# Optimization experiments

Hardware: AMD Instinct MI355X
Metric: run time of the kernel (lower is better)

The kernel has to match this reference:

```python
import jax, jax.numpy as jnp
import numpy as np
from jax import lax


def conv2d(x, w, pad):
    return lax.conv_general_dilated(x, w, (1, 1), [(pad, pad), (pad, pad)],
                                    dimension_numbers=('NCHW', 'OIHW', 'NCHW'))


def deform_conv2d(x, offset, w, b, k, pad):
    # torchvision-style DeformConv2d, stride 1, dilation 1, 1 group.
    # offset: [B, 2*k*k, H, W], pairs ordered (dy, dx) per kernel tap (row-major).
    B, C, H, W = x.shape
    KK = k * k
    off = offset.reshape(B, KK, 2, H, W)
    ky, kx = jnp.meshgrid(jnp.arange(k), jnp.arange(k), indexing='ij')
    ky = ky.reshape(1, KK, 1, 1).astype(x.dtype)
    kx = kx.reshape(1, KK, 1, 1).astype(x.dtype)
    gy = jnp.arange(H, dtype=x.dtype).reshape(1, 1, H, 1)
    gx = jnp.arange(W, dtype=x.dtype).reshape(1, 1, 1, W)
    ys = gy + ky - pad + off[:, :, 0]  # [B, KK, H, W]
    xs = gx + kx - pad + off[:, :, 1]
    y0 = jnp.floor(ys)
    x0 = jnp.floor(xs)
    y1 = y0 + 1.0
    x1 = x0 + 1.0
    img = x.reshape(B, C, H * W)

    def corner(yc, xc, wt):
        # zero padding outside the image
        valid = (yc >= 0) & (yc <= H - 1) & (xc >= 0) & (xc <= W - 1)
        idx = (jnp.clip(yc, 0, H - 1) * W + jnp.clip(xc, 0, W - 1)).astype(jnp.int32).reshape(B, -1)
        g = jax.vmap(lambda im, ix: jnp.take(im, ix, axis=1))(img, idx)  # [B, C, KK*H*W]
        return g.reshape(B, C, KK, H, W) * (wt * valid)[:, None]

    v = (corner(y0, x0, (y1 - ys) * (x1 - xs))
         + corner(y0, x1, (y1 - ys) * (xs - x0))
         + corner(y1, x0, (ys - y0) * (x1 - xs))
         + corner(y1, x1, (ys - y0) * (xs - x0)))  # [B, C, KK, H, W]
    out = jnp.einsum('bckhw,ock->bohw', v, w.reshape(w.shape[0], C, KK))
    return out + b[None, :, None, None]


def setup_inputs() -> dict:
    key = jax.random.key(0)
    ks = jax.random.split(key, 16)
    f32 = jnp.float32
    dim = 64

    def rn(k, shape, s):
        return jax.random.normal(k, shape, f32) * s

    return {
        'x': rn(ks[0], (4, dim, 96, 96), 1.0),
        'w_off3': rn(ks[1], (18, dim, 3, 3), 0.01), 'b_off3': jnp.zeros((18,), f32),
        'w_off5': rn(ks[2], (50, dim, 3, 3), 0.01), 'b_off5': jnp.zeros((50,), f32),
        'w_off7': rn(ks[3], (98, dim, 3, 3), 0.01), 'b_off7': jnp.zeros((98,), f32),
        'w_d3': rn(ks[4], (dim, dim, 3, 3), 0.04), 'b_d3': rn(ks[5], (dim,), 0.01),
        'w_d5': rn(ks[6], (dim, dim, 5, 5), 0.025), 'b_d5': rn(ks[7], (dim,), 0.01),
        'w_d7': rn(ks[8], (dim, dim, 7, 7), 0.018), 'b_d7': rn(ks[9], (dim,), 0.01),
        'w_sp': rn(ks[10], (1, 2, 7, 7), 0.1),
        'w_ca1': rn(ks[11], (12, 3 * dim, 1, 1), 0.07),
        'w_ca2': rn(ks[12], (3 * dim, 12, 1, 1), 0.28),
    }


def reference(x, w_off3, b_off3, w_off5, b_off5, w_off7, b_off7,
              w_d3, b_d3, w_d5, b_d5, w_d7, b_d7, w_sp, w_ca1, w_ca2):
    off3 = conv2d(x, w_off3, 1) + b_off3[None, :, None, None]
    off5 = conv2d(x, w_off5, 1) + b_off5[None, :, None, None]
    off7 = conv2d(x, w_off7, 1) + b_off7[None, :, None, None]
    a1 = deform_conv2d(x, off3, w_d3, b_d3, 3, 1)
    a2 = deform_conv2d(x, off5, w_d5, b_d5, 5, 2)
    a3 = deform_conv2d(x, off7, w_d7, b_d7, 7, 3)
    res = jnp.concatenate([a1, a2, a3], axis=1)  # [B, 3C, H, W]

    # SpatialAttention: channel mean/max -> 7x7 conv -> sigmoid
    sp_in = jnp.concatenate([jnp.mean(res, axis=1, keepdims=True),
                             jnp.max(res, axis=1, keepdims=True)], axis=1)
    sp = jax.nn.sigmoid(conv2d(sp_in, w_sp, 3))  # [B, 1, H, W]

    # ChannelAttention: shared MLP on avg- and max-pooled descriptors
    def fc(t):
        return conv2d(jnp.maximum(conv2d(t, w_ca1, 0), 0.0), w_ca2, 0)

    avg = jnp.mean(res, axis=(2, 3), keepdims=True)
    mx = jnp.max(res, axis=(2, 3), keepdims=True)
    ch = jax.nn.sigmoid(fc(avg) + fc(mx))  # [B, 3C, 1, 1]

    C = x.shape[1]
    c1, c2, c3 = ch[:, :C], ch[:, C:2 * C], ch[:, 2 * C:]
    return a1 * (sp + c1) + a2 * (sp + c2) + a3 * (sp + c3)
```

## Files before the change

### kernel.cpp

```cpp
#include <hip/hip_runtime.h>
#include <math.h>

#define H 96
#define W 96
#define HW (H*W)
#define CIN 64
#define NB 4
#define NOFF 166
#define OFFROW 168

typedef __attribute__((ext_vector_type(8)))  short short8;
typedef __attribute__((ext_vector_type(8)))  _Float16 half8;
typedef __attribute__((ext_vector_type(16))) float f32x16;
typedef unsigned short ushort_t;

static const size_t OFF_ALL = 0;
static const size_t RES     = OFF_ALL + (size_t)NB*HW*OFFROW;
static const size_t XB16    = RES + (size_t)NB*192*HW;
static const size_t WTD3    = XB16 + (size_t)NB*64*HW/2;
static const size_t WTD5    = WTD3 + 9*4096/2;
static const size_t WTD7    = WTD5 + 25*4096/2;
static const size_t WOFF    = WTD7 + 49*4096/2;
static const size_t BOFF    = WOFF + 9*192*64/2;
static const size_t SPIN    = BOFF + 192;
static const size_t SPATT   = SPIN + (size_t)NB*2*HW;
static const size_t POOLAVG = SPATT + (size_t)NB*HW;
static const size_t POOLMAX = POOLAVG + NB*192;
static const size_t CHATT   = POOLMAX + NB*192;

__device__ __forceinline__ ushort_t f2h(float f) {
    _Float16 h = (_Float16)f;
    return __builtin_bit_cast(unsigned short, h);
}
__device__ __forceinline__ half8 as_h8(short8 s) {
    return __builtin_bit_cast(half8, s);
}
__device__ __forceinline__ half8 splat8(float f) {
    _Float16 h = (_Float16)f;
    half8 v;
    #pragma unroll
    for (int j = 0; j < 8; j++) v[j] = h;
    return v;
}

__global__ __launch_bounds__(256) void convert_x_nhwc_kernel(const float* __restrict__ x,
                                                             ushort_t* __restrict__ xb) {
    __shared__ ushort_t tile[64][66];
    int t = threadIdx.x;
    int b = blockIdx.x / 144;
    int p0 = (blockIdx.x % 144) * 64;
    int q = t >> 6, ln = t & 63;
    #pragma unroll
    for (int i = 0; i < 16; i++) {
        int c = q * 16 + i;
        tile[ln][c] = f2h(x[((size_t)(b * 64 + c)) * HW + p0 + ln]);
    }
    __syncthreads();
    #pragma unroll
    for (int i = 0; i < 16; i++) {
        int pos = q * 16 + i;
        xb[((size_t)b * HW + p0 + pos) * 64 + ln] = tile[pos][ln];
    }
}

__global__ void convert_weights_kernel(const float* __restrict__ w3, const float* __restrict__ w5,
                                       const float* __restrict__ w7,
                                       const float* __restrict__ ob3, const float* __restrict__ ob5,
                                       const float* __restrict__ ob7,
                                       const float* __restrict__ ow3, const float* __restrict__ ow5,
                                       const float* __restrict__ ow7,
                                       ushort_t* __restrict__ wt3, ushort_t* __restrict__ wt5,
                                       ushort_t* __restrict__ wt7,
                                       ushort_t* __restrict__ woff, float* __restrict__ boff) {
    int idx = blockIdx.x * 256 + threadIdx.x;
    if (idx < 83 * 4096) {
        const float* src; ushort_t* dst; int KK; int o;
        if (idx < 9 * 4096)       { src = w3; dst = wt3; KK = 9;  o = idx; }
        else if (idx < 34 * 4096) { src = w5; dst = wt5; KK = 25; o = idx - 9 * 4096; }
        else                      { src = w7; dst = wt7; KK = 49; o = idx - 34 * 4096; }
        int j    = o & 7;
        int l31  = (o >> 3) & 31;
        int lh   = (o >> 8) & 1;
        int cs   = (o >> 9) & 3;
        int half = (o >> 11) & 1;
        int kk   = o >> 12;
        int co = half * 32 + l31;
        int c  = cs * 16 + lh * 8 + j;
        dst[o] = f2h(src[((size_t)co * 64 + c) * KK + kk]);
        return;
    }
    int o = idx - 83 * 4096;
    if (o >= 9 * 192 * 64) return;
    int c  = o & 63;
    int co = (o >> 6) % 192;
    int kk = o / (192 * 64);
    float v = 0.f;
    if (co < 18)       v = ow3[(co * 64 + c) * 9 + kk];
    else if (co < 68)  v = ow5[((co - 18) * 64 + c) * 9 + kk];
    else if (co < 166) v = ow7[((co - 68) * 64 + c) * 9 + kk];
    woff[(kk * 192 + co) * 64 + c] = f2h(v);
    if (kk == 0 && c == 0) {
        float bv = 0.f;
        if (co < 18)       bv = ob3[co];
        else if (co < 68)  bv = ob5[co - 18];
        else if (co < 166) bv = ob7[co - 68];
        boff[co] = bv;
    }
}

__global__ __launch_bounds__(256, 3) void offset_mfma_kernel(
    const ushort_t* __restrict__ xb,
    const ushort_t* __restrict__ woff,
    const float* __restrict__ bias_all,
    float* __restrict__ off_all)
{
    __shared__ float red[6144];
    const int t = threadIdx.x;
    const int lane = t & 63, l31 = lane & 31, lh = lane >> 5;
    const int wave = t >> 6;
    const int mhalf = wave >> 1, khalf = wave & 1;
    const int xcd = blockIdx.x & 7, u = blockIdx.x >> 3;
    const int b = xcd >> 1;
    const int v = u * 2 + (xcd & 1);
    const int npos = v * 32 + l31;
    const int h = npos / 96, w = npos % 96;
    const int c0 = 8 * lh;
    const ushort_t* xbase = xb + (size_t)b * HW * 64;

    f32x16 acc0, acc1, acc2;
    #pragma unroll
    for (int r = 0; r < 16; r++) { acc0[r] = 0.f; acc1[r] = 0.f; acc2[r] = 0.f; }

    const int kk0 = khalf ? 5 : 0, kk1 = khalf ? 9 : 5;
    const int mt0 = mhalf * 3;
    for (int kk = kk0; kk < kk1; kk++) {
        int ky = kk / 3, kx = kk % 3;
        int y = h + ky - 1, x = w + kx - 1;
        bool ok = ((unsigned)y < (unsigned)H) && ((unsigned)x < (unsigned)W);
        int o = ok ? (y * W + x) : 0;
        short zm = ok ? (short)0xFFFF : (short)0;
        const ushort_t* px = xbase + (size_t)o * 64 + c0;
        const ushort_t* wk = woff + (size_t)kk * 12288;
        #pragma unroll
        for (int cs = 0; cs < 4; cs++) {
            int cc = cs * 16;
            short8 q = *(const short8*)(px + cc);
            short8 bm;
            #pragma unroll
            for (int j = 0; j < 8; j++) bm[j] = (short)(q[j] & zm);
            half8 bfrag = as_h8(bm);
            half8 a0 = as_h8(*(const short8*)(wk + (size_t)((mt0 + 0) * 32 + l31) * 64 + cc + c0));
            half8 a1 = as_h8(*(const short8*)(wk + (size_t)((mt0 + 1) * 32 + l31) * 64 + cc + c0));
            half8 a2 = as_h8(*(const short8*)(wk + (size_t)((mt0 + 2) * 32 + l31) * 64 + cc + c0));
            acc0 = __builtin_amdgcn_mfma_f32_32x32x16_f16(a0, bfrag, acc0, 0, 0, 0);
            acc1 = __builtin_amdgcn_mfma_f32_32x32x16_f16(a1, bfrag, acc1, 0, 0, 0);
            acc2 = __builtin_amdgcn_mfma_f32_32x32x16_f16(a2, bfrag, acc2, 0, 0, 0);
        }
    }

    if (khalf) {
        float* rp = red + mhalf * 3072;
        #pragma unroll
        for (int r = 0; r < 16; r++) {
            rp[(0 * 16 + r) * 64 + lane] = acc0[r];
            rp[(1 * 16 + r) * 64 + lane] = acc1[r];
            rp[(2 * 16 + r) * 64 + lane] = acc2[r];
        }
    }
    __syncthreads();
    if (!khalf) {
        const float* rp = red + mhalf * 3072;
        #pragma unroll
        for (int r = 0; r < 16; r++) {
            acc0[r] += rp[(0 * 16 + r) * 64 + lane];
            acc1[r] += rp[(1 * 16 + r) * 64 + lane];
            acc2[r] += rp[(2 * 16 + r) * 64 + lane];
        }
        float* row = off_all + ((size_t)b * HW + npos) * OFFROW;
        #pragma unroll
        for (int m = 0; m < 3; m++) {
            const f32x16& a = (m == 0) ? acc0 : (m == 1) ? acc1 : acc2;
            int mt = mt0 + m;
            #pragma unroll
            for (int q = 0; q < 4; q++) {
                int base = mt * 32 + 8 * q + 4 * lh;
                if (base < 166) {
                    float4 vv = make_float4(a[4 * q + 0] + bias_all[base + 0],
                                            a[4 * q + 1] + bias_all[base + 1],
                                            a[4 * q + 2] + bias_all[base + 2],
                                            a[4 * q + 3] + bias_all[base + 3]);
                    *(float4*)(row + base) = vv;
                }
            }
        }
    }
}

__device__ __forceinline__ void store_tile(int b, int tile, int lane, int g,
                                           const float* __restrict__ bias,
                                           const f32x16& acc0, const f32x16& acc1,
                                           float* __restrict__ res)
{
    const int l31 = lane & 31, lh = lane >> 5;
    const int npos = tile * 32 + l31;
    size_t rb = (((size_t)b * 3 + g) * 64) * HW + npos;
    #pragma unroll
    for (int r = 0; r < 16; r++) {
        int co = (r & 3) + 8 * (r >> 2) + 4 * lh;
        res[rb + (size_t)co * HW]        = acc0[r] + bias[co];
        res[rb + (size_t)(co + 32) * HW] = acc1[r] + bias[co + 32];
    }
}

#define MG  5
#define PNY 12
#define PNX 43
#define PXS 144
#define PRS (PNX * PXS)

template<int K, int PAD>
__device__ __forceinline__ void deform_span(
    const float* __restrict__ offp, const ushort_t* __restrict__ wtf,
    int kk0, int kk1, int h, int w, int w0, int l31, int lh,
    const char* lds, f32x16& acc0, f32x16& acc1)
{
    const int lh16 = lh * 16;
    const float2* offp2 = (const float2*)offp;
    float2 off = offp2[kk0];
    for (int kk = kk0; kk < kk1; kk++) {
        float2 noff = offp2[(kk + 1 < kk1) ? kk + 1 : kk];

        int ky = kk / K, kx = kk % K;
        float ys = (float)(h + ky - PAD) + off.x;
        float xs = (float)(w + kx - PAD) + off.y;
        float y0f = floorf(ys), x0f = floorf(xs);
        float fy = ys - y0f, fx = xs - x0f;
        int iy0 = (int)y0f, ix0 = (int)x0f;
        int iy1 = iy0 + 1, ix1 = ix0 + 1;
        float oky0 = ((unsigned)iy0 < (unsigned)H) ? 1.f : 0.f;
        float oky1 = ((unsigned)iy1 < (unsigned)H) ? 1.f : 0.f;
        float okx0 = ((unsigned)ix0 < (unsigned)W) ? 1.f : 0.f;
        float okx1 = ((unsigned)ix1 < (unsigned)W) ? 1.f : 0.f;
        float w00 = (1.f - fy) * (1.f - fx) * oky0 * okx0;
        float w01 = (1.f - fy) * fx * oky0 * okx1;
        float w10 = fy * (1.f - fx) * oky1 * okx0;
        float w11 = fy * fx * oky1 * okx1;
        int cy0 = min(max(iy0, 0), H - 1), cy1 = min(max(iy1, 0), H - 1);
        int cx0 = min(max(ix0, 0), W - 1), cx1 = min(max(ix1, 0), W - 1);
        int r0 = min(max(cy0 - h + MG, 0), PNY - 1);
        int r1 = min(max(cy1 - h + MG, 0), PNY - 1);
        int p0 = min(max(cx0 - w0 + MG, 0), PNX - 1);
        int p1 = min(max(cx1 - w0 + MG, 0), PNX - 1);
        const char* b00 = lds + r0 * PRS + p0 * PXS + lh16;
        const char* b01 = lds + r0 * PRS + p1 * PXS + lh16;
        const char* b10 = lds + r1 * PRS + p0 * PXS + lh16;
        const char* b11 = lds + r1 * PRS + p1 * PXS + lh16;

        half8 W00 = splat8(w00), W01 = splat8(w01);
        half8 W10 = splat8(w10), W11 = splat8(w11);
        const ushort_t* wkf = wtf + (size_t)kk * 4096;
        #pragma unroll
        for (int cs = 0; cs < 4; cs++) {
            half8 q00 = *(const half8*)(b00 + cs * 32);
            half8 q01 = *(const half8*)(b01 + cs * 32);
            half8 q10 = *(const half8*)(b10 + cs * 32);
            half8 q11 = *(const half8*)(b11 + cs * 32);
            half8 bfrag = q00 * W00 + q01 * W01 + q10 * W10 + q11 * W11;
            half8 a0 = as_h8(*(const short8*)(wkf + (size_t)(((0 * 4 + cs) * 2 + lh) * 32 + l31) * 8));
            half8 a1 = as_h8(*(const short8*)(wkf + (size_t)(((1 * 4 + cs) * 2 + lh) * 32 + l31) * 8));
            acc0 = __builtin_amdgcn_mfma_f32_32x32x16_f16(a0, bfrag, acc0, 0, 0, 0);
            acc1 = __builtin_amdgcn_mfma_f32_32x32x16_f16(a1, bfrag, acc1, 0, 0, 0);
        }
        off = noff;
    }
}

__global__ __launch_bounds__(256, 2) void deform_fused_kernel(
    const ushort_t* __restrict__ xb, const float* __restrict__ off_all,
    const ushort_t* __restrict__ wt3, const ushort_t* __restrict__ wt5,
    const ushort_t* __restrict__ wt7,
    const float* __restrict__ b3, const float* __restrict__ b5,
    const float* __restrict__ b7,
    float* __restrict__ res)
{
    __shared__ __align__(16) char lds[PNY * PNX * PXS];
    const int t = threadIdx.x;
    const int wave = t >> 6, lane = t & 63;
    const int xcd = blockIdx.x & 7, u = blockIdx.x >> 3;
    const int b = xcd >> 1;
    const int tile = u * 2 + (xcd & 1);

    const int l31 = lane & 31, lh = lane >> 5;
    const int h  = tile / 3;
    const int w0 = (tile % 3) * 32;
    const int w  = w0 + l31;
    const int npos = h * 96 + w;

    const ushort_t* xsrc = xb + (size_t)b * HW * 64;
    constexpr int NCH = PNY * PNX * 8;
    constexpr int NITER = (NCH + 255) / 256;
    #pragma unroll
    for (int it = 0; it < NITER; it++) {
        int c = t + it * 256;
        if (c < NCH) {
            int rr  = c / (PNX * 8);
            int rem = c - rr * (PNX * 8);
            int pp  = rem >> 3, sub = rem & 7;
            int cy = min(max(h - MG + rr, 0), H - 1);
            int cx = min(max(w0 - MG + pp, 0), W - 1);
            *(float4*)(lds + rr * PRS + pp * PXS + sub * 16) =
                *(const float4*)(xsrc + ((size_t)(cy * W + cx)) * 64 + sub * 8);
        }
    }
    __syncthreads();

    const float* offrow = off_all + ((size_t)b * HW + npos) * OFFROW;

    f32x16 a0A, a1A, a0B, a1B;
    #pragma unroll
    for (int r = 0; r < 16; r++) { a0A[r] = 0.f; a1A[r] = 0.f; a0B[r] = 0.f; a1B[r] = 0.f; }

    if (wave == 0) {
        deform_span<3, 1>(offrow + 0,  wt3, 0, 9,  h, w, w0, l31, lh, lds, a0A, a1A);
        deform_span<5, 2>(offrow + 18, wt5, 0, 12, h, w, w0, l31, lh, lds, a0B, a1B);
    } else if (wave == 1) {
        deform_span<5, 2>(offrow + 18, wt5, 12, 25, h, w, w0, l31, lh, lds, a0A, a1A);
        deform_span<7, 3>(offrow + 68, wt7, 0, 8,   h, w, w0, l31, lh, lds, a0B, a1B);
    } else if (wave == 2) {
        deform_span<7, 3>(offrow + 68, wt7, 8, 29,  h, w, w0, l31, lh, lds, a0A, a1A);
    } else {
        deform_span<7, 3>(offrow + 68, wt7, 29, 49, h, w, w0, l31, lh, lds, a0A, a1A);
    }

    __syncthreads();
    float* slots = (float*)lds;
    if (wave == 1) {
        float* s0 = slots;
        float* s1 = slots + 2048;
        #pragma unroll
        for (int r = 0; r < 16; r++) {
            s0[r * 64 + lane]        = a0A[r];
            s0[(16 + r) * 64 + lane] = a1A[r];
            s1[r * 64 + lane]        = a0B[r];
            s1[(16 + r) * 64 + lane] = a1B[r];
        }
    } else if (wave == 3) {
        float* s2 = slots + 4096;
        #pragma unroll
        for (int r = 0; r < 16; r++) {
            s2[r * 64 + lane]        = a0A[r];
            s2[(16 + r) * 64 + lane] = a1A[r];
        }
    }
    __syncthreads();
    if (wave == 0) {
        store_tile(b, tile, lane, 0, b3, a0A, a1A, res);
        const float* s0 = slots;
        #pragma unroll
        for (int r = 0; r < 16; r++) {
            a0B[r] += s0[r * 64 + lane];
            a1B[r] += s0[(16 + r) * 64 + lane];
        }
        store_tile(b, tile, lane, 1, b5, a0B, a1B, res);
    } else if (wave == 2) {
        const float* s1 = slots + 2048;
        const float* s2 = slots + 4096;
        #pragma unroll
        for (int r = 0; r < 16; r++) {
            a0A[r] += s1[r * 64 + lane] + s2[r * 64 + lane];
            a1A[r] += s1[(16 + r) * 64 + lane] + s2[(16 + r) * 64 + lane];
        }
        store_tile(b, tile, lane, 2, b7, a0A, a1A, res);
    }
}

__global__ void sp_meanmax_kernel(const float* __restrict__ res,
                                  float* __restrict__ spin) {
    int gt  = blockIdx.x * 256 + threadIdx.x;
    int idx = gt >> 2;
    int q   = gt & 3;
    int hw = idx % HW;
    int b  = idx / HW;
    const float* r = res + ((size_t)b * 192 + q * 48) * HW + hw;
    float s = 0.f, m = -3.402823466e+38f;
    for (int c = 0; c < 48; c++) {
        float v = r[(size_t)c * HW];
        s += v;
        m = fmaxf(m, v);
    }
    s += __shfl_xor(s, 1);  m = fmaxf(m, __shfl_xor(m, 1));
    s += __shfl_xor(s, 2);  m = fmaxf(m, __shfl_xor(m, 2));
    if (q == 0) {
        spin[(size_t)b * 2 * HW + hw]      = s * (1.f / 192.f);
        spin[(size_t)b * 2 * HW + HW + hw] = m;
    }
}

__global__ void sp_conv_kernel(const float* __restrict__ spin,
                               const float* __restrict__ w_sp,
                               float* __restrict__ sp) {
    int gt  = blockIdx.x * 256 + threadIdx.x;
    int idx = gt >> 2;
    int q   = gt & 3;
    int w = idx % W;
    int h = (idx / W) % H;
    int b = idx / HW;
    int ci  = q >> 1;
    int dy0 = (q & 1) ? 4 : 0;
    int dy1 = (q & 1) ? 7 : 4;
    const float* pin = spin + ((size_t)b * 2 + ci) * HW;
    const float* wp  = w_sp + ci * 49;
    float acc = 0.f;
    for (int dy = dy0; dy < dy1; dy++) {
        int yy = h + dy - 3;
        if (yy < 0 || yy >= H) continue;
        #pragma unroll
        for (int dx = 0; dx < 7; dx++) {
            int xx = w + dx - 3;
            if (xx < 0 || xx >= W) continue;
            acc = fmaf(pin[yy * W + xx], wp[dy * 7 + dx], acc);
        }
    }
    acc += __shfl_xor(acc, 1);
    acc += __shfl_xor(acc, 2);
    if (q == 0) sp[idx] = 1.f / (1.f + expf(-acc));
}

__global__ void pool_kernel(const float* __restrict__ res,
                            float* __restrict__ avg, float* __restrict__ mx) {
    int bc = blockIdx.x;
    const float* r = res + (size_t)bc * HW;
    int t = threadIdx.x;
    float s = 0.f, m = -3.402823466e+38f;
    for (int i = t; i < HW; i += 256) {
        float v = r[i];
        s += v;
        m = fmaxf(m, v);
    }
    #pragma unroll
    for (int off = 32; off > 0; off >>= 1) {
        s += __shfl_down(s, off);
        m = fmaxf(m, __shfl_down(m, off));
    }
    __shared__ float ss[4], sm[4];
    int wid = t >> 6;
    if ((t & 63) == 0) { ss[wid] = s; sm[wid] = m; }
    __syncthreads();
    if (t == 0) {
        s = ss[0] + ss[1] + ss[2] + ss[3];
        m = fmaxf(fmaxf(sm[0], sm[1]), fmaxf(sm[2], sm[3]));
        avg[bc] = s * (1.f / (float)HW);
        mx[bc]  = m;
    }
}

__global__ void chatt_kernel(const float* __restrict__ avg,
                             const float* __restrict__ mx,
                             const float* __restrict__ w1,
                             const float* __restrict__ w2,
                             float* __restrict__ ch) {
    int b = blockIdx.x;
    int t = threadIdx.x;
    __shared__ float sa[192], sm_[192], h1a[12], h1m[12];
    if (t < 192) { sa[t] = avg[b * 192 + t]; sm_[t] = mx[b * 192 + t]; }
    __syncthreads();
    if (t < 192) {
        int j = t >> 4, lg = t & 15;
        float s1 = 0.f, s2 = 0.f;
        #pragma unroll
        for (int i = 0; i < 12; i++) {
            int c = lg + i * 16;
            float wv = w1[j * 192 + c];
            s1 = fmaf(wv, sa[c], s1);
            s2 = fmaf(wv, sm_[c], s2);
        }
        #pragma unroll
        for (int d = 1; d < 16; d <<= 1) {
            s1 += __shfl_xor(s1, d);
            s2 += __shfl_xor(s2, d);
        }
        if (lg == 0) {
            h1a[j] = fmaxf(s1, 0.f);
            h1m[j] = fmaxf(s2, 0.f);
        }
    }
    __syncthreads();
    if (t < 192) {
        float s = 0.f;
        #pragma unroll
        for (int j = 0; j < 12; j++)
            s = fmaf(w2[t * 12 + j], h1a[j] + h1m[j], s);
        ch[b * 192 + t] = 1.f / (1.f + expf(-s));
    }
}

__global__ void final_kernel(const float* __restrict__ res,
                             const float* __restrict__ sp,
                             const float* __restrict__ ch,
                             float* __restrict__ out) {
    int idx = blockIdx.x * 256 + threadIdx.x;
    int hw = idx % HW;
    int co = (idx / HW) % 64;
    int b  = idx / (64 * HW);
    size_t rb = (size_t)b * 192 * HW;
    float a1 = res[rb + (size_t)co * HW + hw];
    float a2 = res[rb + (size_t)(64 + co) * HW + hw];
    float a3 = res[rb + (size_t)(128 + co) * HW + hw];
    float spv = sp[(size_t)b * HW + hw];
    float c1 = ch[b * 192 + co];
    float c2 = ch[b * 192 + 64 + co];
    float c3 = ch[b * 192 + 128 + co];
    out[idx] = a1 * (spv + c1) + a2 * (spv + c2) + a3 * (spv + c3);
}

extern "C" void kernel_launch(void* const* d_in, const int* in_sizes, int n_in,
                              void* d_out, int out_size, void* d_ws, size_t ws_size,
                              hipStream_t stream) {
    const float* x      = (const float*)d_in[0];
    const float* w_off3 = (const float*)d_in[1];
    const float* b_off3 = (const float*)d_in[2];
    const float* w_off5 = (const float*)d_in[3];
    const float* b_off5 = (const float*)d_in[4];
    const float* w_off7 = (const float*)d_in[5];
    const float* b_off7 = (const float*)d_in[6];
    const float* w_d3   = (const float*)d_in[7];
    const float* b_d3   = (const float*)d_in[8];
    const float* w_d5   = (const float*)d_in[9];
    const float* b_d5   = (const float*)d_in[10];
    const float* w_d7   = (const float*)d_in[11];
    const float* b_d7   = (const float*)d_in[12];
    const float* w_sp   = (const float*)d_in[13];
    const float* w_ca1  = (const float*)d_in[14];
    const float* w_ca2  = (const float*)d_in[15];

    float* ws = (float*)d_ws;
    float* off_all = ws + OFF_ALL;
    float* res     = ws + RES;
    ushort_t* xb16 = (ushort_t*)(ws + XB16);
    ushort_t* wt3  = (ushort_t*)(ws + WTD3);
    ushort_t* wt5  = (ushort_t*)(ws + WTD5);
    ushort_t* wt7  = (ushort_t*)(ws + WTD7);
    ushort_t* woff = (ushort_t*)(ws + WOFF);
    float* boff = ws + BOFF;
    float* spin = ws + SPIN;
    float* sp   = ws + SPATT;
    float* avgp = ws + POOLAVG;
    float* mxp  = ws + POOLMAX;
    float* chp  = ws + CHATT;

    convert_x_nhwc_kernel<<<576, 256, 0, stream>>>(x, xb16);
    convert_weights_kernel<<<1760, 256, 0, stream>>>(w_d3, w_d5, w_d7,
                                                     b_off3, b_off5, b_off7,
                                                     w_off3, w_off5, w_off7,
                                                     wt3, wt5, wt7, woff, boff);

    offset_mfma_kernel<<<1152, 256, 0, stream>>>(xb16, woff, boff, off_all);

    deform_fused_kernel<<<1152, 256, 0, stream>>>(xb16, off_all, wt3, wt5, wt7,
                                                  b_d3, b_d5, b_d7, res);

    sp_meanmax_kernel<<<576, 256, 0, stream>>>(res, spin);
    sp_conv_kernel<<<576, 256, 0, stream>>>(spin, w_sp, sp);
    pool_kernel<<<768, 256, 0, stream>>>(res, avgp, mxp);
    chatt_kernel<<<4, 256, 0, stream>>>(avgp, mxp, w_ca1, w_ca2, chp);

    final_kernel<<<9216, 256, 0, stream>>>(res, sp, chp, (float*)d_out);
}
```

Measured before the change: 158.2 us.

## Add zero pad pixel, raise MFMA priority, vectorize final combine with float4

Each batch of the fp16 NHWC input now gets one extra zeroed pixel, so out-of-bounds taps in the offset conv read that pixel instead of masking the loaded values. MFMA issue priority is raised with s_setprio around the deform-conv matrix ops to favour them over the gather work. The final attention-combine kernel is vectorized to float4 loads and stores with a quarter of the blocks. Together these cut masking ALU work and memory instruction count, at the cost of slightly more workspace and a layout change every consumer of the converted input must follow.

```diff
diff --git a/kernel.cpp b/kernel.cpp
--- a/kernel.cpp
+++ b/kernel.cpp
@@ -8,6 +8,7 @@
 #define NB 4
 #define NOFF 166
 #define OFFROW 168
+#define HWP (HW+1)
 
 typedef __attribute__((ext_vector_type(8)))  short short8;
 typedef __attribute__((ext_vector_type(8)))  _Float16 half8;
@@ -17,7 +18,7 @@
 static const size_t OFF_ALL = 0;
 static const size_t RES     = OFF_ALL + (size_t)NB*HW*OFFROW;
 static const size_t XB16    = RES + (size_t)NB*192*HW;
-static const size_t WTD3    = XB16 + (size_t)NB*64*HW/2;
+static const size_t WTD3    = XB16 + (size_t)NB*64*HWP/2;
 static const size_t WTD5    = WTD3 + 9*4096/2;
 static const size_t WTD7    = WTD5 + 25*4096/2;
 static const size_t WOFF    = WTD7 + 49*4096/2;
@@ -55,11 +56,12 @@
         int c = q * 16 + i;
         tile[ln][c] = f2h(x[((size_t)(b * 64 + c)) * HW + p0 + ln]);
     }
+    if (p0 == 0 && t < 64) xb[((size_t)b * HWP + HW) * 64 + t] = 0;
     __syncthreads();
     #pragma unroll
     for (int i = 0; i < 16; i++) {
         int pos = q * 16 + i;
-        xb[((size_t)b * HW + p0 + pos) * 64 + ln] = tile[pos][ln];
+        xb[((size_t)b * HWP + p0 + pos) * 64 + ln] = tile[pos][ln];
     }
 }
 
@@ -125,7 +127,7 @@
     const int npos = v * 32 + l31;
     const int h = npos / 96, w = npos % 96;
     const int c0 = 8 * lh;
-    const ushort_t* xbase = xb + (size_t)b * HW * 64;
+    const ushort_t* xbase = xb + (size_t)b * HWP * 64;
 
     f32x16 acc0, acc1, acc2;
     #pragma unroll
@@ -137,18 +139,13 @@
         int ky = kk / 3, kx = kk % 3;
         int y = h + ky - 1, x = w + kx - 1;
         bool ok = ((unsigned)y < (unsigned)H) && ((unsigned)x < (unsigned)W);
-        int o = ok ? (y * W + x) : 0;
-        short zm = ok ? (short)0xFFFF : (short)0;
+        int o = ok ? (y * W + x) : HW;
         const ushort_t* px = xbase + (size_t)o * 64 + c0;
         const ushort_t* wk = woff + (size_t)kk * 12288;
         #pragma unroll
         for (int cs = 0; cs < 4; cs++) {
             int cc = cs * 16;
-            short8 q = *(const short8*)(px + cc);
-            short8 bm;
-            #pragma unroll
-            for (int j = 0; j < 8; j++) bm[j] = (short)(q[j] & zm);
-            half8 bfrag = as_h8(bm);
+            half8 bfrag = as_h8(*(const short8*)(px + cc));
             half8 a0 = as_h8(*(const short8*)(wk + (size_t)((mt0 + 0) * 32 + l31) * 64 + cc + c0));
             half8 a1 = as_h8(*(const short8*)(wk + (size_t)((mt0 + 1) * 32 + l31) * 64 + cc + c0));
             half8 a2 = as_h8(*(const short8*)(wk + (size_t)((mt0 + 2) * 32 + l31) * 64 + cc + c0));
@@ -268,8 +265,10 @@
             half8 bfrag = q00 * W00 + q01 * W01 + q10 * W10 + q11 * W11;
             half8 a0 = as_h8(*(const short8*)(wkf + (size_t)(((0 * 4 + cs) * 2 + lh) * 32 + l31) * 8));
             half8 a1 = as_h8(*(const short8*)(wkf + (size_t)(((1 * 4 + cs) * 2 + lh) * 32 + l31) * 8));
+            __builtin_amdgcn_s_setprio(1);
             acc0 = __builtin_amdgcn_mfma_f32_32x32x16_f16(a0, bfrag, acc0, 0, 0, 0);
             acc1 = __builtin_amdgcn_mfma_f32_32x32x16_f16(a1, bfrag, acc1, 0, 0, 0);
+            __builtin_amdgcn_s_setprio(0);
         }
         off = noff;
     }
@@ -296,7 +295,7 @@
     const int w  = w0 + l31;
     const int npos = h * 96 + w;
 
-    const ushort_t* xsrc = xb + (size_t)b * HW * 64;
+    const ushort_t* xsrc = xb + (size_t)b * HWP * 64;
     constexpr int NCH = PNY * PNX * 8;
     constexpr int NITER = (NCH + 255) / 256;
     #pragma unroll
@@ -499,18 +498,23 @@
                              const float* __restrict__ ch,
                              float* __restrict__ out) {
     int idx = blockIdx.x * 256 + threadIdx.x;
-    int hw = idx % HW;
-    int co = (idx / HW) % 64;
-    int b  = idx / (64 * HW);
-    size_t rb = (size_t)b * 192 * HW;
-    float a1 = res[rb + (size_t)co * HW + hw];
-    float a2 = res[rb + (size_t)(64 + co) * HW + hw];
-    float a3 = res[rb + (size_t)(128 + co) * HW + hw];
-    float spv = sp[(size_t)b * HW + hw];
+    int hw4 = idx % (HW / 4);
+    int co  = (idx / (HW / 4)) % 64;
+    int b   = idx / (64 * (HW / 4));
+    size_t rb = (size_t)b * 192 * HW + (size_t)co * HW + hw4 * 4;
+    float4 a1 = *(const float4*)(res + rb);
+    float4 a2 = *(const float4*)(res + rb + (size_t)64 * HW);
+    float4 a3 = *(const float4*)(res + rb + (size_t)128 * HW);
+    float4 spv = *(const float4*)(sp + (size_t)b * HW + hw4 * 4);
     float c1 = ch[b * 192 + co];
     float c2 = ch[b * 192 + 64 + co];
     float c3 = ch[b * 192 + 128 + co];
-    out[idx] = a1 * (spv + c1) + a2 * (spv + c2) + a3 * (spv + c3);
+    float4 o;
+    o.x = a1.x * (spv.x + c1) + a2.x * (spv.x + c2) + a3.x * (spv.x + c3);
+    o.y = a1.y * (spv.y + c1) + a2.y * (spv.y + c2) + a3.y * (spv.y + c3);
+    o.z = a1.z * (spv.z + c1) + a2.z * (spv.z + c2) + a3.z * (spv.z + c3);
+    o.w = a1.w * (spv.w + c1) + a2.w * (spv.w + c2) + a3.w * (spv.w + c3);
+    *(float4*)(out + ((size_t)b * 64 + co) * HW + hw4 * 4) = o;
 }
 
 extern "C" void kernel_launch(void* const* d_in, const int* in_sizes, int n_in,
@@ -564,5 +568,5 @@
     pool_kernel<<<768, 256, 0, stream>>>(res, avgp, mxp);
     chatt_kernel<<<4, 256, 0, stream>>>(avgp, mxp, w_ca1, w_ca2, chp);
 
-    final_kernel<<<9216, 256, 0, stream>>>(res, sp, chp, (float*)d_out);
-}
+    final_kernel<<<2304, 256, 0, stream>>>(res, sp, chp, (float*)d_out);
+}
```

New measurement: 187.2 us. +18.3%, slower.
